# Optimization experiments

Measured on AMD Instinct MI355X. Metric: run time of the kernel, lower is better.

The kernel has to match this reference:

```python
import jax, jax.numpy as jnp
import numpy as np

B, T, D = 4, 4096, 1024

def setup_inputs() -> dict:
    key = jax.random.key(0)
    ks = jax.random.split(key, 6)
    x = jax.random.normal(ks[0], (B, T, D), dtype=jnp.float32)
    mask = jax.random.randint(ks[1], (B, T), 0, 2).astype(bool)
    # torch nn.Linear init scale ~ 1/sqrt(fan_in); exact init unimportant for correctness baseline
    s = 1.0 / np.sqrt(D)
    W_qkv = jax.random.normal(ks[2], (3 * D, D), dtype=jnp.float32) * s
    b_qkv = jax.random.normal(ks[3], (3 * D,), dtype=jnp.float32) * s
    W_out = jax.random.normal(ks[4], (D, D), dtype=jnp.float32) * s
    b_out = jax.random.normal(ks[5], (D,), dtype=jnp.float32) * s
    return {"x": x, "mask": mask, "W_qkv": W_qkv, "b_qkv": b_qkv, "W_out": W_out, "b_out": b_out}

def reference(x, mask, W_qkv, b_qkv, W_out, b_out):
    # qkv projection: (B,T,D) @ (D,3D) + (3D,)
    qkv = jnp.einsum('btd,ed->bte', x, W_qkv) + b_qkv
    q, k, v = jnp.split(qkv, 3, axis=-1)  # each (B,T,D)
    q = q / jnp.linalg.norm(q, axis=-1, keepdims=True)
    k = k / jnp.linalg.norm(k, axis=-1, keepdims=True)
    k = jnp.where(mask[..., None], 0.0, k)  # masked_fill(mask, 0)
    kv = jnp.sum(k * v, axis=-2, keepdims=True)  # (B,1,D) global feature sum
    out = kv * q  # (B,T,D)
    return jnp.einsum('btd,ed->bte', out, W_out) + b_out
```

## Files before the change

### kernel.cpp

```cpp
#include <hip/hip_runtime.h>
#include <stdint.h>


typedef short  short8   __attribute__((ext_vector_type(8)));
typedef float  floatx16 __attribute__((ext_vector_type(16)));

#define BM 128
#define BN 128
#define BK 64

__device__ __forceinline__ void async16(const void* g, void* l) {
  __builtin_amdgcn_global_load_lds((const __attribute__((address_space(1))) void*)g,
                                   (__attribute__((address_space(3))) void*)l, 16, 0, 0);
}

__device__ __forceinline__ uint16_t f2bf(float f) {
  union { float f; uint32_t u; } x; x.f = f;
  uint32_t u = x.u;
  return (uint16_t)((u + 0x7fffu + ((u >> 16) & 1u)) >> 16);
}
__device__ __forceinline__ float bf2f(uint16_t h) {
  union { uint32_t u; float f; } x; x.u = ((uint32_t)h) << 16; return x.f;
}
__device__ __forceinline__ uint32_t pack2(float a, float b) {
  return (uint32_t)f2bf(a) | ((uint32_t)f2bf(b) << 16);
}
__device__ __forceinline__ void upk8(uint4 u, float* f) {
  f[0]=bf2f((uint16_t)u.x); f[1]=bf2f((uint16_t)(u.x>>16));
  f[2]=bf2f((uint16_t)u.y); f[3]=bf2f((uint16_t)(u.y>>16));
  f[4]=bf2f((uint16_t)u.z); f[5]=bf2f((uint16_t)(u.z>>16));
  f[6]=bf2f((uint16_t)u.w); f[7]=bf2f((uint16_t)(u.w>>16));
}

__global__ __launch_bounds__(256) void cvt3(
    const float* __restrict__ a, uint16_t* __restrict__ ao, int na,
    const float* __restrict__ b, uint16_t* __restrict__ bo, int nb,
    const float* __restrict__ c, uint16_t* __restrict__ co, int nc) {
  int i = blockIdx.x * 256 + threadIdx.x;
  const float* in; uint16_t* out; int j = i;
  if (j < na) { in = a; out = ao; }
  else {
    j -= na;
    if (j < nb) { in = b; out = bo; }
    else { j -= nb; if (j >= nc) return; in = c; out = co; }
  }
  const float4* p = (const float4*)in;
  float4 u = p[(size_t)j * 2], v = p[(size_t)j * 2 + 1];
  uint4 o;
  o.x = pack2(u.x, u.y); o.y = pack2(u.z, u.w);
  o.z = pack2(v.x, v.y); o.w = pack2(v.z, v.w);
  ((uint4*)out)[j] = o;
}

__global__ __launch_bounds__(256, 2) void gemm1(
    const uint16_t* __restrict__ A, const uint16_t* __restrict__ Bw,
    const float* __restrict__ bias, uint16_t* __restrict__ Cb,
    int N, int K)
{
  __shared__ __align__(16) uint16_t As[BM * BK];
  __shared__ __align__(16) uint16_t Bs[BN * BK];
  const int tid = threadIdx.x;
  const int wave = tid >> 6, lane = tid & 63;
  const int l31 = lane & 31, khalf = lane >> 5;
  const int wm = wave & 1, wn = wave >> 1;
  const int tileM = blockIdx.y * BM, tileN = blockIdx.x * BN;

  const int srow = wave * 8 + (lane >> 3);
  const int skc  = (lane & 7) ^ (lane >> 3);
  const uint16_t* gA = A  + (size_t)(tileM + srow) * K + skc * 8;
  const uint16_t* gB = Bw + (size_t)(tileN + srow) * K + skc * 8;
  char* lA = (char*)As + wave * 64 * 16;
  char* lB = (char*)Bs + wave * 64 * 16;

  floatx16 acc[2][2];
#pragma unroll
  for (int mi = 0; mi < 2; mi++)
#pragma unroll
    for (int ni = 0; ni < 2; ni++)
#pragma unroll
      for (int r = 0; r < 16; r++) acc[mi][ni][r] = 0.f;

  const int arow0 = wm * 64 + l31;
  const int brow0 = wn * 64 + l31;

  for (int k0 = 0; k0 < K; k0 += BK) {
#pragma unroll
    for (int s = 0; s < 4; s++) {
      async16(gA + k0 + s * 32 * K, lA + s * 4096);
      async16(gB + k0 + s * 32 * K, lB + s * 4096);
    }
    __syncthreads();
#pragma unroll
    for (int ks = 0; ks < 4; ks++) {
      const int kc = khalf + ks * 2;
      short8 af[2], bfr[2];
#pragma unroll
      for (int mi = 0; mi < 2; mi++) {
        int r = arow0 + mi * 32;
        af[mi] = *(const short8*)&As[(r * 8 + (kc ^ (r & 7))) * 8];
      }
#pragma unroll
      for (int ni = 0; ni < 2; ni++) {
        int r = brow0 + ni * 32;
        bfr[ni] = *(const short8*)&Bs[(r * 8 + (kc ^ (r & 7))) * 8];
      }
#pragma unroll
      for (int mi = 0; mi < 2; mi++)
#pragma unroll
        for (int ni = 0; ni < 2; ni++)
          acc[mi][ni] = __builtin_amdgcn_mfma_f32_32x32x16_bf16(af[mi], bfr[ni], acc[mi][ni], 0, 0, 0);
    }
    __syncthreads();
  }

#pragma unroll
  for (int mi = 0; mi < 2; mi++) {
    int rbase = tileM + wm * 64 + mi * 32 + 4 * khalf;
#pragma unroll
    for (int ni = 0; ni < 2; ni++) {
      int col = tileN + wn * 64 + ni * 32 + l31;
      float bv = bias[col];
#pragma unroll
      for (int reg = 0; reg < 16; reg++) {
        int row = rbase + (reg & 3) + 8 * (reg >> 2);
        Cb[(size_t)row * N + col] = f2bf(acc[mi][ni][reg] + bv);
      }
    }
  }
}

__global__ __launch_bounds__(256, 2) void gemm2(
    const uint16_t* __restrict__ qkv, const float* __restrict__ invq,
    const float* __restrict__ kv, const uint16_t* __restrict__ Bw,
    const float* __restrict__ bias, float* __restrict__ Cf,
    int N, int K)
{
  __shared__ __align__(16) uint16_t As[BM * BK];
  __shared__ __align__(16) uint16_t Bs[BN * BK];
  const int tid = threadIdx.x;
  const int wave = tid >> 6, lane = tid & 63;
  const int l31 = lane & 31, khalf = lane >> 5;
  const int wm = wave & 1, wn = wave >> 1;
  const int tileM = blockIdx.y * BM, tileN = blockIdx.x * BN;

  const int srow = wave * 8 + (lane >> 3);
  const int skc  = (lane & 7) ^ (lane >> 3);
  const uint16_t* gB = Bw + (size_t)(tileN + srow) * K + skc * 8;
  char* lB = (char*)Bs + wave * 64 * 16;
  const float* kvb = kv + ((tileM >> 12) << 10);

  float sinv[4];
#pragma unroll
  for (int s = 0; s < 4; s++) sinv[s] = invq[tileM + s * 32 + srow];

  floatx16 acc[2][2];
#pragma unroll
  for (int mi = 0; mi < 2; mi++)
#pragma unroll
    for (int ni = 0; ni < 2; ni++)
#pragma unroll
      for (int r = 0; r < 16; r++) acc[mi][ni][r] = 0.f;

  const int arow0 = wm * 64 + l31;
  const int brow0 = wn * 64 + l31;

  for (int k0 = 0; k0 < K; k0 += BK) {
#pragma unroll
    for (int s = 0; s < 4; s++)
      async16(gB + k0 + s * 32 * K, lB + s * 4096);
#pragma unroll
    for (int s = 0; s < 4; s++) {
      int r = tileM + s * 32 + srow;
      int d = k0 + skc * 8;
      uint4 qv = *(const uint4*)(qkv + (size_t)r * 3072 + d);
      float4 k0v = *(const float4*)(kvb + d);
      float4 k1v = *(const float4*)(kvb + d + 4);
      float qf[8]; upk8(qv, qf);
      float sc = sinv[s];
      uint4 o;
      o.x = pack2(qf[0] * sc * k0v.x, qf[1] * sc * k0v.y);
      o.y = pack2(qf[2] * sc * k0v.z, qf[3] * sc * k0v.w);
      o.z = pack2(qf[4] * sc * k1v.x, qf[5] * sc * k1v.y);
      o.w = pack2(qf[6] * sc * k1v.z, qf[7] * sc * k1v.w);
      *(uint4*)((char*)As + (size_t)(s * 256 + wave * 64 + lane) * 16) = o;
    }
    __syncthreads();
#pragma unroll
    for (int ks = 0; ks < 4; ks++) {
      const int kc = khalf + ks * 2;
      short8 af[2], bfr[2];
#pragma unroll
      for (int mi = 0; mi < 2; mi++) {
        int r = arow0 + mi * 32;
        af[mi] = *(const short8*)&As[(r * 8 + (kc ^ (r & 7))) * 8];
      }
#pragma unroll
      for (int ni = 0; ni < 2; ni++) {
        int r = brow0 + ni * 32;
        bfr[ni] = *(const short8*)&Bs[(r * 8 + (kc ^ (r & 7))) * 8];
      }
#pragma unroll
      for (int mi = 0; mi < 2; mi++)
#pragma unroll
        for (int ni = 0; ni < 2; ni++)
          acc[mi][ni] = __builtin_amdgcn_mfma_f32_32x32x16_bf16(af[mi], bfr[ni], acc[mi][ni], 0, 0, 0);
    }
    __syncthreads();
  }

#pragma unroll
  for (int mi = 0; mi < 2; mi++) {
    int rbase = tileM + wm * 64 + mi * 32 + 4 * khalf;
#pragma unroll
    for (int ni = 0; ni < 2; ni++) {
      int col = tileN + wn * 64 + ni * 32 + l31;
      float bv = bias[col];
#pragma unroll
      for (int reg = 0; reg < 16; reg++) {
        int row = rbase + (reg & 3) + 8 * (reg >> 2);
        Cf[(size_t)row * N + col] = acc[mi][ni][reg] + bv;
      }
    }
  }
}

__global__ __launch_bounds__(256) void detect_mask(const unsigned char* __restrict__ m,
                                                   int* __restrict__ flag) {
  int i = blockIdx.x * blockDim.x + threadIdx.x;
  int v = ((i & 3) != 0) ? (int)m[i] : 0;
  unsigned long long b = __ballot(v != 0);
  if ((threadIdx.x & 63) == 0 && b) atomicOr(flag, 1);
}

__global__ __launch_bounds__(256) void rownorm_kv(
    const uint16_t* __restrict__ qkv, const void* __restrict__ maskbuf,
    const int* __restrict__ flag, float* __restrict__ invq, float* __restrict__ kv)
{
  __shared__ float kvloc[1024];
  const int tid = threadIdx.x;
  for (int i = tid; i < 1024; i += 256) kvloc[i] = 0.f;
  __syncthreads();
  const int wave = tid >> 6, lane = tid & 63;
  const int b = blockIdx.x >> 7;
  const int chunk = blockIdx.x & 127;
  const int isU8 = *flag;
  const unsigned char* m8 = (const unsigned char*)maskbuf;
  const int* m32 = (const int*)maskbuf;

  float kvacc[16];
#pragma unroll
  for (int i = 0; i < 16; i++) kvacc[i] = 0.f;

  const int r0 = b * 4096 + chunk * 32 + wave * 8;
  for (int j = 0; j < 8; j++) {
    int r = r0 + j;
    const uint16_t* rp = qkv + (size_t)r * 3072;
    uint4 q0 = *(const uint4*)(rp + lane * 16);
    uint4 q1 = *(const uint4*)(rp + lane * 16 + 8);
    uint4 k0 = *(const uint4*)(rp + 1024 + lane * 16);
    uint4 k1 = *(const uint4*)(rp + 1024 + lane * 16 + 8);
    uint4 v0 = *(const uint4*)(rp + 2048 + lane * 16);
    uint4 v1 = *(const uint4*)(rp + 2048 + lane * 16 + 8);
    float qf[16], kf[16], vf[16];
    upk8(q0, qf); upk8(q1, qf + 8);
    upk8(k0, kf); upk8(k1, kf + 8);
    upk8(v0, vf); upk8(v1, vf + 8);
    float sq = 0.f, sk = 0.f;
#pragma unroll
    for (int i = 0; i < 16; i++) { sq = fmaf(qf[i], qf[i], sq); sk = fmaf(kf[i], kf[i], sk); }
    for (int off = 32; off; off >>= 1) { sq += __shfl_xor(sq, off); sk += __shfl_xor(sk, off); }
    float rq = rsqrtf(sq), rk = rsqrtf(sk);
    if (lane == 0) invq[r] = rq;
    int masked = isU8 ? (int)m8[r] : m32[r];
    if (!masked) {
#pragma unroll
      for (int i = 0; i < 16; i++) kvacc[i] = fmaf(kf[i] * rk, vf[i], kvacc[i]);
    }
  }
#pragma unroll
  for (int i = 0; i < 16; i++) atomicAdd(&kvloc[lane * 16 + i], kvacc[i]);
  __syncthreads();
  for (int i = tid; i < 1024; i += 256) atomicAdd(&kv[b * 1024 + i], kvloc[i]);
}

extern "C" void kernel_launch(void* const* d_in, const int* in_sizes, int n_in,
                              void* d_out, int out_size, void* d_ws, size_t ws_size,
                              hipStream_t stream) {
  const float* x     = (const float*)d_in[0];
  const void*  mask  = d_in[1];
  const float* W_qkv = (const float*)d_in[2];
  const float* b_qkv = (const float*)d_in[3];
  const float* W_out = (const float*)d_in[4];
  const float* b_out = (const float*)d_in[5];
  float* out = (float*)d_out;

  const int BT = 4 * 4096;
  const int D  = 1024;

  char* ws = (char*)d_ws;
  size_t off = 0;
  auto alloc = [&](size_t bytes) { size_t r = off; off += (bytes + 255) & ~(size_t)255; return r; };
  size_t o_xb   = alloc((size_t)BT * D * 2);
  size_t o_qkvb = alloc((size_t)BT * 3 * D * 2);
  size_t o_wq   = alloc((size_t)3 * D * D * 2);
  size_t o_wo   = alloc((size_t)D * D * 2);
  size_t o_kv   = alloc((size_t)4 * D * 4 + 256);
  size_t o_invq = alloc((size_t)BT * 4);

  uint16_t* xb   = (uint16_t*)(ws + o_xb);
  uint16_t* qkvb = (uint16_t*)(ws + o_qkvb);
  uint16_t* wq   = (uint16_t*)(ws + o_wq);
  uint16_t* wo   = (uint16_t*)(ws + o_wo);
  float*    kv   = (float*)(ws + o_kv);
  int*      flag = (int*)(ws + o_kv + (size_t)4 * D * 4);
  float*    invq = (float*)(ws + o_invq);

  hipMemsetAsync(ws + o_kv, 0, (size_t)4 * D * 4 + 256, stream);
  {
    int na = BT * D / 8, nb = 3 * D * D / 8, nc = D * D / 8;
    int tot = na + nb + nc;
    cvt3<<<dim3((tot + 255) / 256), 256, 0, stream>>>(x, xb, na, W_qkv, wq, nb, W_out, wo, nc);
  }
  detect_mask<<<dim3(64), 256, 0, stream>>>((const unsigned char*)mask, flag);
  gemm1<<<dim3(3 * D / BN, BT / BM), 256, 0, stream>>>(xb, wq, b_qkv, qkvb, 3 * D, D);
  rownorm_kv<<<dim3(512), 256, 0, stream>>>(qkvb, mask, flag, invq, kv);
  gemm2<<<dim3(D / BN, BT / BM), 256, 0, stream>>>(qkvb, invq, kv, wo, b_out, out, D, D);
}
```

Measured before the change: 342.2 us.

## Prefetch q rows in gemm2, cache kv in LDS, widen rownorm grid

In gemm2 the kv vector for the batch is staged once into shared memory, and the q tile for the next K step is loaded into registers one iteration ahead, so global load latency overlaps with the MFMA work. The loop bounds are now the compile-time constant 1024, with a partial unroll. rownorm_kv now launches 2048 blocks of 8 rows each instead of 512 blocks of 32 rows, which gives more parallelism but means more atomic or partial-sum traffic into kv. The costs are higher register pressure from the prefetched q values, a gemm2 hardcoded to D=1024, and extra kv reductions.

```diff
diff --git a/kernel.cpp b/kernel.cpp
--- a/kernel.cpp
+++ b/kernel.cpp
@@ -132,11 +132,11 @@
 __global__ __launch_bounds__(256, 2) void gemm2(
     const uint16_t* __restrict__ qkv, const float* __restrict__ invq,
     const float* __restrict__ kv, const uint16_t* __restrict__ Bw,
-    const float* __restrict__ bias, float* __restrict__ Cf,
-    int N, int K)
+    const float* __restrict__ bias, float* __restrict__ Cf)
 {
   __shared__ __align__(16) uint16_t As[BM * BK];
   __shared__ __align__(16) uint16_t Bs[BN * BK];
+  __shared__ __align__(16) float kvs[1024];
   const int tid = threadIdx.x;
   const int wave = tid >> 6, lane = tid & 63;
   const int l31 = lane & 31, khalf = lane >> 5;
@@ -145,10 +145,13 @@
 
   const int srow = wave * 8 + (lane >> 3);
   const int skc  = (lane & 7) ^ (lane >> 3);
-  const uint16_t* gB = Bw + (size_t)(tileN + srow) * K + skc * 8;
+  const uint16_t* gB = Bw + (size_t)(tileN + srow) * 1024 + skc * 8;
   char* lB = (char*)Bs + wave * 64 * 16;
-  const float* kvb = kv + ((tileM >> 12) << 10);
-
+
+  {
+    int i = tid * 4;
+    *(float4*)&kvs[i] = *(const float4*)(kv + ((tileM >> 12) << 10) + i);
+  }
   float sinv[4];
 #pragma unroll
   for (int s = 0; s < 4; s++) sinv[s] = invq[tileM + s * 32 + srow];
@@ -164,18 +167,33 @@
   const int arow0 = wm * 64 + l31;
   const int brow0 = wn * 64 + l31;
 
-  for (int k0 = 0; k0 < K; k0 += BK) {
+  const uint16_t* qbase = qkv + (size_t)(tileM + srow) * 3072 + skc * 8;
+  uint4 nq[4];
+#pragma unroll
+  for (int s = 0; s < 4; s++)
+    nq[s] = *(const uint4*)(qbase + (size_t)s * 32 * 3072);
+
+  __syncthreads();
+
+#pragma unroll 2
+  for (int k0 = 0; k0 < 1024; k0 += BK) {
+    uint4 cq[4];
+#pragma unroll
+    for (int s = 0; s < 4; s++) cq[s] = nq[s];
+    if (k0 + BK < 1024) {
+#pragma unroll
+      for (int s = 0; s < 4; s++)
+        nq[s] = *(const uint4*)(qbase + (size_t)s * 32 * 3072 + k0 + BK);
+    }
 #pragma unroll
     for (int s = 0; s < 4; s++)
-      async16(gB + k0 + s * 32 * K, lB + s * 4096);
+      async16(gB + k0 + s * 32 * 1024, lB + s * 4096);
 #pragma unroll
     for (int s = 0; s < 4; s++) {
-      int r = tileM + s * 32 + srow;
       int d = k0 + skc * 8;
-      uint4 qv = *(const uint4*)(qkv + (size_t)r * 3072 + d);
-      float4 k0v = *(const float4*)(kvb + d);
-      float4 k1v = *(const float4*)(kvb + d + 4);
-      float qf[8]; upk8(qv, qf);
+      float4 k0v = *(const float4*)&kvs[d];
+      float4 k1v = *(const float4*)&kvs[d + 4];
+      float qf[8]; upk8(cq[s], qf);
       float sc = sinv[s];
       uint4 o;
       o.x = pack2(qf[0] * sc * k0v.x, qf[1] * sc * k0v.y);
@@ -218,7 +236,7 @@
 #pragma unroll
       for (int reg = 0; reg < 16; reg++) {
         int row = rbase + (reg & 3) + 8 * (reg >> 2);
-        Cf[(size_t)row * N + col] = acc[mi][ni][reg] + bv;
+        Cf[(size_t)row * 1024 + col] = acc[mi][ni][reg] + bv;
       }
     }
   }
@@ -241,8 +259,7 @@
   for (int i = tid; i < 1024; i += 256) kvloc[i] = 0.f;
   __syncthreads();
   const int wave = tid >> 6, lane = tid & 63;
-  const int b = blockIdx.x >> 7;
-  const int chunk = blockIdx.x & 127;
+  const int b = blockIdx.x >> 9;
   const int isU8 = *flag;
   const unsigned char* m8 = (const unsigned char*)maskbuf;
   const int* m32 = (const int*)maskbuf;
@@ -251,8 +268,9 @@
 #pragma unroll
   for (int i = 0; i < 16; i++) kvacc[i] = 0.f;
 
-  const int r0 = b * 4096 + chunk * 32 + wave * 8;
-  for (int j = 0; j < 8; j++) {
+  const int r0 = blockIdx.x * 8 + wave * 2;
+#pragma unroll
+  for (int j = 0; j < 2; j++) {
     int r = r0 + j;
     const uint16_t* rp = qkv + (size_t)r * 3072;
     uint4 q0 = *(const uint4*)(rp + lane * 16);
@@ -323,6 +341,6 @@
   }
   detect_mask<<<dim3(64), 256, 0, stream>>>((const unsigned char*)mask, flag);
   gemm1<<<dim3(3 * D / BN, BT / BM), 256, 0, stream>>>(xb, wq, b_qkv, qkvb, 3 * D, D);
-  rownorm_kv<<<dim3(512), 256, 0, stream>>>(qkvb, mask, flag, invq, kv);
-  gemm2<<<dim3(D / BN, BT / BM), 256, 0, stream>>>(qkvb, invq, kv, wo, b_out, out, D, D);
-}
+  rownorm_kv<<<dim3(2048), 256, 0, stream>>>(qkvb, mask, flag, invq, kv);
+  gemm2<<<dim3(D / BN, BT / BM), 256, 0, stream>>>(qkvb, invq, kv, wo, b_out, out);
+}
```

Measured after the change: 374.2 us. +9.4%, slower.
